# Kernel optimization log

Measured on AMD Instinct MI355X. Metric: run time of the kernel, lower is better.

The kernel has to match this reference:

```python
import jax, jax.numpy as jnp
import numpy as np


def setup_inputs() -> dict:
    key = jax.random.key(0)
    ks = jax.random.split(key, 5)
    B, S, D, H = 2, 2048, 1024, 16
    dk = D // H
    scale = D ** -0.5
    x = jax.random.normal(ks[0], (B, S, D), dtype=jnp.float32)
    W_Q = scale * jax.random.normal(ks[1], (H, D, dk), dtype=jnp.float32)
    W_K = scale * jax.random.normal(ks[2], (H, D, dk), dtype=jnp.float32)
    W_V = scale * jax.random.normal(ks[3], (H, D, dk), dtype=jnp.float32)
    W_O = scale * jax.random.normal(ks[4], (H * dk, D), dtype=jnp.float32)
    return {"x": x, "W_Q": W_Q, "W_K": W_K, "W_V": W_V, "W_O": W_O}


def reference(x, W_Q, W_K, W_V, W_O):
    # x: [B,S,D]; W_Q/W_K/W_V: [H,D,dk]; W_O: [H*dk, D]
    dk = W_Q.shape[-1]
    Q = jnp.einsum('bsd,hdk->bhsk', x, W_Q)
    K = jnp.einsum('bsd,hdk->bhsk', x, W_K)
    V = jnp.einsum('bsd,hdk->bhsk', x, W_V)
    scores = jnp.einsum('bhqk,bhsk->bhqs', Q, K) / jnp.sqrt(jnp.float32(dk))
    attn = jax.nn.softmax(scores, axis=-1)
    heads = jnp.einsum('bhqs,bhsk->bhqk', attn, V)  # [B,H,S,dk]
    B, H, S, _ = heads.shape
    concat = heads.transpose(0, 2, 1, 3).reshape(B, S, H * dk)  # [B,S,H*dk]
    return concat @ W_O
```

## Files before the change

### kernel.cpp

```cpp
#include <hip/hip_runtime.h>

typedef __attribute__((ext_vector_type(8))) short bf16x8;
typedef __attribute__((ext_vector_type(4))) float f32x4;
typedef __attribute__((ext_vector_type(4))) unsigned short u16x4;
typedef unsigned short u16;
typedef unsigned int u32;

static __device__ __forceinline__ u16 f2bf(float f) {
  u32 u = __float_as_uint(f);
  u32 r = (u + 0x7fffu + ((u >> 16) & 1u)) >> 16;
  return (u16)r;
}

static __device__ __forceinline__ u32 cvt_pk(float lo, float hi) {
  u32 r;
  asm("v_cvt_pk_bf16_f32 %0, %1, %2" : "=v"(r) : "v"(lo), "v"(hi));
  return r;
}

#define GLDS16(g, l)                                                        \
  __builtin_amdgcn_global_load_lds(                                         \
      (const __attribute__((address_space(1))) u32*)(g),                    \
      (__attribute__((address_space(3))) u32*)(l), 16, 0, 0)

#define WAIT_VM0() asm volatile("s_waitcnt vmcnt(0)" ::: "memory")
#define RAWBAR() __builtin_amdgcn_s_barrier()

#define SC2F 0.18033688011112042f

__global__ __launch_bounds__(256) void cast_all(const float* __restrict__ x,
                                                const float* __restrict__ wq,
                                                const float* __restrict__ wk,
                                                const float* __restrict__ wv,
                                                const float* __restrict__ wo,
                                                u16* __restrict__ xb,
                                                u16* __restrict__ wqkv,
                                                u16* __restrict__ wot) {
  __shared__ u16 tile[64][66];
  int bid = blockIdx.x, t = threadIdx.x;
  if (bid < 2048) {
    int i = bid * 256 + t;
    const float4* xv = (const float4*)x;
    float4 a = xv[i * 2], b = xv[i * 2 + 1];
    bf16x8 o;
    o[0] = f2bf(a.x); o[1] = f2bf(a.y); o[2] = f2bf(a.z); o[3] = f2bf(a.w);
    o[4] = f2bf(b.x); o[5] = f2bf(b.y); o[6] = f2bf(b.z); o[7] = f2bf(b.w);
    *(bf16x8*)(xb + i * 8) = o;
    return;
  }
  const float* src;
  u16* dstb;
  if (bid < 2816) {
    int id = bid - 2048;
    int dt = id & 15, h = (id >> 4) & 15, sel = id >> 8;
    src = (sel == 0 ? wq : (sel == 1 ? wk : wv)) + h * 65536 + dt * 4096;
    dstb = wqkv + ((size_t)(h * 192 + sel * 64)) * 1024 + dt * 64;
    int r = t >> 4, c4 = (t & 15) * 4;
#pragma unroll
    for (int p = 0; p < 4; ++p) {
      int rr = r + p * 16;
      float4 v = *(const float4*)(src + rr * 64 + c4);
      u16x4 o;
      o[0] = f2bf(v.x); o[1] = f2bf(v.y); o[2] = f2bf(v.z); o[3] = f2bf(v.w);
      *(u16x4*)&tile[rr][c4] = o;
    }
  } else {
    int id = bid - 2816;
    int nt = id & 15, kt = id >> 4;
    src = wo + (size_t)(kt * 64) * 1024 + nt * 64;
    dstb = wot + (size_t)(nt * 64) * 1024 + kt * 64;
    int r = t >> 4, c4 = (t & 15) * 4;
#pragma unroll
    for (int p = 0; p < 4; ++p) {
      int rr = r + p * 16;
      float4 v = *(const float4*)(src + (size_t)rr * 1024 + c4);
      u16x4 o;
      o[0] = f2bf(v.x); o[1] = f2bf(v.y); o[2] = f2bf(v.z); o[3] = f2bf(v.w);
      *(u16x4*)&tile[rr][c4] = o;
    }
  }
  __syncthreads();
  int nn = t >> 3, dc = (t & 7) * 8;
#pragma unroll
  for (int p = 0; p < 2; ++p) {
    int np = nn + p * 32;
    u16x4 a, b2;
#pragma unroll
    for (int i = 0; i < 4; ++i) {
      a[i] = tile[dc + i][np];
      b2[i] = tile[dc + 4 + i][np];
    }
    *(u16x4*)(dstb + (size_t)np * 1024 + dc) = a;
    *(u16x4*)(dstb + (size_t)np * 1024 + dc + 4) = b2;
  }
}

__global__ __launch_bounds__(256) void gemm_qkv(const u16* __restrict__ A,
                                                const u16* __restrict__ Bt,
                                                u16* __restrict__ qkb,
                                                u16* __restrict__ Vt, int M,
                                                int N, int K) {
  const int t = threadIdx.x;
  const int lane = t & 63, w = t >> 6;
  const int lr = lane & 15, lg = lane >> 4;
  const int wr = w >> 1, wc = w & 1;
  int lin = blockIdx.y * gridDim.x + blockIdx.x;
  int bx = 2 * (lin & 7) + ((lin >> 3) & 1);
  int by = lin >> 4;
  const int m0 = by * 128, n0 = bx * 192, head = bx;
  __shared__ __align__(16) u16 SM[40960];
  const int rs = t >> 3, cs = t & 7;
  const int sw = (cs ^ (rs & 7)) * 8;
  const u16* a0 = A + (size_t)(m0 + rs) * K + sw;
  const u16* b0 = Bt + (size_t)(n0 + rs) * K + sw;
  int chk[2];
#pragma unroll
  for (int kk = 0; kk < 2; ++kk) chk[kk] = ((kk * 4 + lg) ^ (lr & 7)) * 8;
  f32x4 acc[4][6] = {};

#define QSTAGE(bb, k0)                                                     \
  {                                                                        \
    _Pragma("unroll") for (int p = 0; p < 4; ++p)                          \
        GLDS16(a0 + (size_t)p * 32 * K + (k0),                             \
               &SM[(bb)*8192 + (p * 256 + t) * 8]);                        \
    _Pragma("unroll") for (int p = 0; p < 6; ++p)                          \
        GLDS16(b0 + (size_t)p * 32 * K + (k0),                             \
               &SM[16384 + (bb)*12288 + (p * 256 + t) * 8]);               \
  }

  QSTAGE(0, 0);
  for (int k0 = 0; k0 < K; k0 += 64) {
    const int bb = (k0 >> 6) & 1;
    WAIT_VM0();
    RAWBAR();
    if (k0 + 64 < K) QSTAGE(bb ^ 1, k0 + 64);
#pragma unroll
    for (int kk = 0; kk < 2; ++kk) {
      bf16x8 a[4], b[6];
#pragma unroll
      for (int m = 0; m < 4; ++m)
        a[m] = *(const bf16x8*)&SM[bb * 8192 + (wr * 64 + m * 16 + lr) * 64 + chk[kk]];
#pragma unroll
      for (int n = 0; n < 6; ++n)
        b[n] = *(const bf16x8*)&SM[16384 + bb * 12288 +
                                   (wc * 96 + n * 16 + lr) * 64 + chk[kk]];
      __builtin_amdgcn_s_setprio(1);
#pragma unroll
      for (int m = 0; m < 4; ++m)
#pragma unroll
        for (int n = 0; n < 6; ++n)
          acc[m][n] =
              __builtin_amdgcn_mfma_f32_16x16x32_bf16(a[m], b[n], acc[m][n], 0, 0, 0);
      __builtin_amdgcn_s_setprio(0);
    }
  }
#undef QSTAGE

#pragma unroll
  for (int m = 0; m < 4; ++m) {
    int rowg = m0 + wr * 64 + m * 16 + lg * 4;
#pragma unroll
    for (int n = 0; n < 6; ++n) {
      int cg = wc * 96 + n * 16 + lr;
      if (cg < 64) {
        int col = head * 64 + cg;
#pragma unroll
        for (int j = 0; j < 4; ++j)
          qkb[(size_t)(rowg + j) * 2048 + col] = f2bf(acc[m][n][j] * SC2F);
      } else if (cg < 128) {
        int col = 1024 + head * 64 + (cg - 64);
#pragma unroll
        for (int j = 0; j < 4; ++j)
          qkb[(size_t)(rowg + j) * 2048 + col] = f2bf(acc[m][n][j]);
      }
    }
  }
  __syncthreads();
  if (wc == 1) {
#pragma unroll
    for (int m = 0; m < 4; ++m)
#pragma unroll
      for (int n = 2; n < 6; ++n) {
        int v = (n - 2) * 16 + lr;
        int s = wr * 64 + m * 16 + lg * 4;
        u16x4 pk;
#pragma unroll
        for (int j = 0; j < 4; ++j) pk[j] = f2bf(acc[m][n][j]);
        *(u16x4*)&SM[v * 136 + s] = pk;
      }
  }
  __syncthreads();
  const int bb2 = m0 >> 11, s0g = m0 & 2047;
  u16* vdst = Vt + ((size_t)(bb2 * 1024 + head * 64)) * 2048 + s0g;
#pragma unroll
  for (int q = 0; q < 4; ++q) {
    int id = q * 256 + t;
    int v = id >> 4, sc = id & 15;
    bf16x8 row = *(const bf16x8*)&SM[v * 136 + sc * 8];
    *(bf16x8*)(vdst + (size_t)v * 2048 + sc * 8) = row;
  }
}

__global__ __launch_bounds__(256) void gemm_out(const u16* __restrict__ A,
                                                const u16* __restrict__ Bt,
                                                float* __restrict__ C, int M,
                                                int N, int K) {
  const int t = threadIdx.x;
  const int lane = t & 63, w = t >> 6;
  const int lr = lane & 15, lg = lane >> 4;
  const int wr = w >> 1, wc = w & 1;
  int lin = blockIdx.y * gridDim.x + blockIdx.x;
  int nwg = gridDim.x * gridDim.y;
  int swz = (lin & 7) * (nwg >> 3) + (lin >> 3);
  int bx = swz % gridDim.x, by = swz / gridDim.x;
  const int m0 = by * 64, n0 = bx * 128;
  __shared__ __align__(16) u16 As[2][64 * 32];
  __shared__ __align__(16) u16 Bs[2][128 * 32];
  const int r0 = t >> 2, cb = (t & 3) * 8;
  const u16* a0 = A + (size_t)(m0 + r0) * K + cb;
  const u16* b0 = Bt + (size_t)(n0 + r0) * K + cb;
  const size_t rowjmp = (size_t)64 * K;
  f32x4 acc[2][4] = {};

#define GSTAGE(bb, k0)                                      \
  {                                                         \
    GLDS16(a0 + (k0), &As[bb][t * 8]);                      \
    GLDS16(b0 + (k0), &Bs[bb][t * 8]);                      \
    GLDS16(b0 + rowjmp + (k0), &Bs[bb][2048 + t * 8]);      \
  }

  GSTAGE(0, 0);
  for (int k0 = 0; k0 < K; k0 += 32) {
    const int bb = (k0 >> 5) & 1;
    WAIT_VM0();
    RAWBAR();
    if (k0 + 32 < K) GSTAGE(bb ^ 1, k0 + 32);
    bf16x8 a[2], b[4];
#pragma unroll
    for (int m = 0; m < 2; ++m)
      a[m] = *(const bf16x8*)&As[bb][(wr * 32 + m * 16 + lr) * 32 + lg * 8];
#pragma unroll
    for (int n = 0; n < 4; ++n)
      b[n] = *(const bf16x8*)&Bs[bb][(wc * 64 + n * 16 + lr) * 32 + lg * 8];
    __builtin_amdgcn_s_setprio(1);
#pragma unroll
    for (int m = 0; m < 2; ++m)
#pragma unroll
      for (int n = 0; n < 4; ++n)
        acc[m][n] =
            __builtin_amdgcn_mfma_f32_16x16x32_bf16(a[m], b[n], acc[m][n], 0, 0, 0);
    __builtin_amdgcn_s_setprio(0);
  }
#undef GSTAGE

#pragma unroll
  for (int m = 0; m < 2; ++m) {
    int rowg = m0 + wr * 32 + m * 16 + lg * 4;
#pragma unroll
    for (int n = 0; n < 4; ++n) {
      int colg = n0 + wc * 64 + n * 16 + lr;
#pragma unroll
      for (int j = 0; j < 4; ++j)
        C[(size_t)(rowg + j) * N + colg] = acc[m][n][j];
    }
  }
}

__global__ __launch_bounds__(256, 2) void attn(const u16* __restrict__ qkb,
                                               const u16* __restrict__ vtb,
                                               u16* __restrict__ hb) {
  const int t = threadIdx.x, lane = t & 63, w = t >> 6;
  const int lr = lane & 15, lg = lane >> 4;
  int lin = blockIdx.x;
  int swz2 = (lin & 7) * 64 + (lin >> 3);
  int qi = swz2 & 15, bh = swz2 >> 4;
  int b = bh >> 4, h = bh & 15;
  int q0 = qi * 128;
  __shared__ __align__(16) u16 Ks[2][128 * 64];
  __shared__ __align__(16) u16 Vts[2][64 * 128];
  __shared__ __align__(16) u32 Ps[4][2][512];

  bf16x8 qf[2][2];
#pragma unroll
  for (int g = 0; g < 2; ++g) {
    const u16* qb =
        qkb + (size_t)(b * 2048 + q0 + w * 32 + g * 16 + lr) * 2048 + h * 64;
    qf[g][0] = *(const bf16x8*)(qb + lg * 8);
    qf[g][1] = *(const bf16x8*)(qb + 32 + lg * 8);
  }
  bf16x8 ones;
#pragma unroll
  for (int i = 0; i < 8; ++i) ones[i] = (short)0x3F80;

  f32x4 oacc[2][4] = {};
  f32x4 le0 = {}, le1 = {};
  float mrun0 = -1e30f, mrun1 = -1e30f;

  int chk[2], chv[4];
#pragma unroll
  for (int kk = 0; kk < 2; ++kk) chk[kk] = ((kk * 4 + lg) ^ (lr & 7)) * 8;
#pragma unroll
  for (int kk = 0; kk < 4; ++kk) chv[kk] = ((kk * 4 + lg) ^ lr) * 8;
  const int xw = (lr & 7) << 2;

  const int rk = t >> 3, ck = t & 7;
  const int rv = t >> 4, cv = t & 15;
  const u16* Kg = qkb + (size_t)(b * 2048) * 2048 + 1024 + h * 64;
  const u16* Vg = vtb + (size_t)(b * 1024 + h * 64) * 2048;
  const u16* kp0 = Kg + (size_t)rk * 2048 + ((ck ^ (rk & 7)) * 8);
  const u16* vp0 = Vg + (size_t)rv * 2048 + ((cv ^ (rv & 15)) * 8);
  u32* Pw0 = &Ps[w][0][0];
  u32* Pw1 = &Ps[w][1][0];

#define ASTAGE(bb, tv)                                 \
  {                                                    \
    const u16* kp = kp0 + (size_t)(tv)*262144;         \
    const u16* vp = vp0 + (tv)*128;                    \
    GLDS16(kp, &Ks[bb][t * 8]);                        \
    GLDS16(kp + 65536, &Ks[bb][2048 + t * 8]);         \
    GLDS16(kp + 131072, &Ks[bb][4096 + t * 8]);        \
    GLDS16(kp + 196608, &Ks[bb][6144 + t * 8]);        \
    GLDS16(vp, &Vts[bb][t * 8]);                       \
    GLDS16(vp + 32768, &Vts[bb][2048 + t * 8]);        \
    GLDS16(vp + 65536, &Vts[bb][4096 + t * 8]);        \
    GLDS16(vp + 98304, &Vts[bb][6144 + t * 8]);        \
  }

  ASTAGE(0, 0);
  for (int tv = 0; tv < 16; ++tv) {
    const int bb = tv & 1;
    WAIT_VM0();
    RAWBAR();
    if (tv < 15) ASTAGE(bb ^ 1, tv + 1);

    f32x4 s0[8], s1[8];
#pragma unroll
    for (int n = 0; n < 8; ++n) {
      s0[n] = (f32x4){0.f, 0.f, 0.f, 0.f};
      s1[n] = (f32x4){0.f, 0.f, 0.f, 0.f};
    }
    __builtin_amdgcn_s_setprio(1);
#pragma unroll
    for (int kk = 0; kk < 2; ++kk)
#pragma unroll
      for (int n = 0; n < 8; ++n) {
        bf16x8 kf = *(const bf16x8*)&Ks[bb][n * 1024 + lr * 64 + chk[kk]];
        s0[n] = __builtin_amdgcn_mfma_f32_16x16x32_bf16(kf, qf[0][kk], s0[n], 0, 0, 0);
        s1[n] = __builtin_amdgcn_mfma_f32_16x16x32_bf16(kf, qf[1][kk], s1[n], 0, 0, 0);
      }
    __builtin_amdgcn_s_setprio(0);

    if ((tv & 3) == 0) {
      float t0[8], t1[8];
#pragma unroll
      for (int n = 0; n < 8; ++n) {
        t0[n] = fmaxf(fmaxf(s0[n][0], s0[n][1]), fmaxf(s0[n][2], s0[n][3]));
        t1[n] = fmaxf(fmaxf(s1[n][0], s1[n][1]), fmaxf(s1[n][2], s1[n][3]));
      }
      float pm0 = fmaxf(fmaxf(fmaxf(t0[0], t0[1]), fmaxf(t0[2], t0[3])),
                        fmaxf(fmaxf(t0[4], t0[5]), fmaxf(t0[6], t0[7])));
      float pm1 = fmaxf(fmaxf(fmaxf(t1[0], t1[1]), fmaxf(t1[2], t1[3])),
                        fmaxf(fmaxf(t1[4], t1[5]), fmaxf(t1[6], t1[7])));
      pm0 = fmaxf(pm0, __shfl_xor(pm0, 16));
      pm0 = fmaxf(pm0, __shfl_xor(pm0, 32));
      pm1 = fmaxf(pm1, __shfl_xor(pm1, 16));
      pm1 = fmaxf(pm1, __shfl_xor(pm1, 32));

      if (__any(fmaxf(pm0 - mrun0, pm1 - mrun1) > 8.0f)) {
        {
          float mn = fmaxf(mrun0, pm0);
          float al = __builtin_amdgcn_exp2f(mrun0 - mn);
          float alj[4];
#pragma unroll
          for (int j = 0; j < 4; ++j) alj[j] = __shfl(al, 4 * lg + j);
#pragma unroll
          for (int j = 0; j < 4; ++j) le0[j] *= alj[j];
#pragma unroll
          for (int n = 0; n < 4; ++n)
#pragma unroll
            for (int j = 0; j < 4; ++j) oacc[0][n][j] *= alj[j];
          mrun0 = mn;
        }
        {
          float mn = fmaxf(mrun1, pm1);
          float al = __builtin_amdgcn_exp2f(mrun1 - mn);
          float alj[4];
#pragma unroll
          for (int j = 0; j < 4; ++j) alj[j] = __shfl(al, 4 * lg + j);
#pragma unroll
          for (int j = 0; j < 4; ++j) le1[j] *= alj[j];
#pragma unroll
          for (int n = 0; n < 4; ++n)
#pragma unroll
            for (int j = 0; j < 4; ++j) oacc[1][n][j] *= alj[j];
          mrun1 = mn;
        }
      }
    }

#pragma unroll
    for (int n = 0; n < 4; ++n) {
      float v0 = __builtin_amdgcn_exp2f(s0[n][0] - mrun0);
      float v1 = __builtin_amdgcn_exp2f(s0[n][1] - mrun0);
      float v2 = __builtin_amdgcn_exp2f(s0[n][2] - mrun0);
      float v3 = __builtin_amdgcn_exp2f(s0[n][3] - mrun0);
      Pw0[lr * 32 + ((8 * n + 2 * lg) ^ xw)] = cvt_pk(v0, v1);
      Pw0[lr * 32 + ((8 * n + 2 * lg + 1) ^ xw)] = cvt_pk(v2, v3);
      float u0 = __builtin_amdgcn_exp2f(s1[n][0] - mrun1);
      float u1 = __builtin_amdgcn_exp2f(s1[n][1] - mrun1);
      float u2 = __builtin_amdgcn_exp2f(s1[n][2] - mrun1);
      float u3 = __builtin_amdgcn_exp2f(s1[n][3] - mrun1);
      Pw1[lr * 32 + ((8 * n + 2 * lg) ^ xw)] = cvt_pk(u0, u1);
      Pw1[lr * 32 + ((8 * n + 2 * lg + 1) ^ xw)] = cvt_pk(u2, u3);
    }
    __builtin_amdgcn_s_setprio(1);
#pragma unroll
    for (int kk = 0; kk < 2; ++kk) {
      bf16x8 pa0 = *(const bf16x8*)&Pw0[lr * 32 + ((16 * kk + 4 * lg) ^ xw)];
      bf16x8 pa1 = *(const bf16x8*)&Pw1[lr * 32 + ((16 * kk + 4 * lg) ^ xw)];
      le0 = __builtin_amdgcn_mfma_f32_16x16x32_bf16(pa0, ones, le0, 0, 0, 0);
      le1 = __builtin_amdgcn_mfma_f32_16x16x32_bf16(pa1, ones, le1, 0, 0, 0);
#pragma unroll
      for (int n = 0; n < 4; ++n) {
        bf16x8 vf = *(const bf16x8*)&Vts[bb][n * 2048 + lr * 128 + chv[kk]];
        oacc[0][n] = __builtin_amdgcn_mfma_f32_16x16x32_bf16(pa0, vf, oacc[0][n], 0, 0, 0);
        oacc[1][n] = __builtin_amdgcn_mfma_f32_16x16x32_bf16(pa1, vf, oacc[1][n], 0, 0, 0);
      }
    }
    __builtin_amdgcn_s_setprio(0);
#pragma unroll
    for (int n = 4; n < 8; ++n) {
      float v0 = __builtin_amdgcn_exp2f(s0[n][0] - mrun0);
      float v1 = __builtin_amdgcn_exp2f(s0[n][1] - mrun0);
      float v2 = __builtin_amdgcn_exp2f(s0[n][2] - mrun0);
      float v3 = __builtin_amdgcn_exp2f(s0[n][3] - mrun0);
      Pw0[lr * 32 + ((8 * (n - 4) + 2 * lg) ^ xw)] = cvt_pk(v0, v1);
      Pw0[lr * 32 + ((8 * (n - 4) + 2 * lg + 1) ^ xw)] = cvt_pk(v2, v3);
      float u0 = __builtin_amdgcn_exp2f(s1[n][0] - mrun1);
      float u1 = __builtin_amdgcn_exp2f(s1[n][1] - mrun1);
      float u2 = __builtin_amdgcn_exp2f(s1[n][2] - mrun1);
      float u3 = __builtin_amdgcn_exp2f(s1[n][3] - mrun1);
      Pw1[lr * 32 + ((8 * (n - 4) + 2 * lg) ^ xw)] = cvt_pk(u0, u1);
      Pw1[lr * 32 + ((8 * (n - 4) + 2 * lg + 1) ^ xw)] = cvt_pk(u2, u3);
    }
    __builtin_amdgcn_s_setprio(1);
#pragma unroll
    for (int kk = 2; kk < 4; ++kk) {
      bf16x8 pa0 = *(const bf16x8*)&Pw0[lr * 32 + ((16 * (kk - 2) + 4 * lg) ^ xw)];
      bf16x8 pa1 = *(const bf16x8*)&Pw1[lr * 32 + ((16 * (kk - 2) + 4 * lg) ^ xw)];
      le0 = __builtin_amdgcn_mfma_f32_16x16x32_bf16(pa0, ones, le0, 0, 0, 0);
      le1 = __builtin_amdgcn_mfma_f32_16x16x32_bf16(pa1, ones, le1, 0, 0, 0);
#pragma unroll
      for (int n = 0; n < 4; ++n) {
        bf16x8 vf = *(const bf16x8*)&Vts[bb][n * 2048 + lr * 128 + chv[kk]];
        oacc[0][n] = __builtin_amdgcn_mfma_f32_16x16x32_bf16(pa0, vf, oacc[0][n], 0, 0, 0);
        oacc[1][n] = __builtin_amdgcn_mfma_f32_16x16x32_bf16(pa1, vf, oacc[1][n], 0, 0, 0);
      }
    }
    __builtin_amdgcn_s_setprio(0);
  }
#undef ASTAGE

  float rj0[4], rj1[4];
#pragma unroll
  for (int j = 0; j < 4; ++j) {
    rj0[j] = __builtin_amdgcn_rcpf(le0[j]);
    rj1[j] = __builtin_amdgcn_rcpf(le1[j]);
  }
  int row0 = b * 2048 + q0 + w * 32 + lg * 4;
#pragma unroll
  for (int n = 0; n < 4; ++n) {
    int col = h * 64 + n * 16 + lr;
#pragma unroll
    for (int j = 0; j < 4; ++j) {
      hb[(size_t)(row0 + j) * 1024 + col] = f2bf(oacc[0][n][j] * rj0[j]);
      hb[(size_t)(row0 + 16 + j) * 1024 + col] = f2bf(oacc[1][n][j] * rj1[j]);
    }
  }
}

extern "C" void kernel_launch(void* const* d_in, const int* in_sizes, int n_in,
                              void* d_out, int out_size, void* d_ws,
                              size_t ws_size, hipStream_t stream) {
  const float* x = (const float*)d_in[0];
  const float* wq = (const float*)d_in[1];
  const float* wk = (const float*)d_in[2];
  const float* wv = (const float*)d_in[3];
  const float* wo = (const float*)d_in[4];

  u16* xb = (u16*)d_ws;
  u16* wqkv = xb + 4 * 1024 * 1024;
  u16* wot = wqkv + 3 * 1024 * 1024;
  u16* qkb = wot + 1024 * 1024;
  u16* vtb = qkb + 8 * 1024 * 1024;
  u16* hb = vtb + 4 * 1024 * 1024;

  cast_all<<<3072, 256, 0, stream>>>(x, wq, wk, wv, wo, xb, wqkv, wot);
  gemm_qkv<<<dim3(16, 32), 256, 0, stream>>>(xb, wqkv, qkb, vtb, 4096, 3072, 1024);
  attn<<<512, 256, 0, stream>>>(qkb, vtb, hb);
  gemm_out<<<dim3(8, 64), 256, 0, stream>>>(hb, wot, (float*)d_out, 4096, 1024, 1024);
}
```

Baseline: 111.4 us.

## Use triple-buffered K=32 stages with partial vmcnt waits in QKV GEMM

New measurement: 112.8 us. Within noise of the previous version (+1.3%).

```diff
diff --git a/kernel.cpp b/kernel.cpp
--- a/kernel.cpp
+++ b/kernel.cpp
@@ -23,6 +23,7 @@
       (const __attribute__((address_space(1))) u32*)(g),                    \
       (__attribute__((address_space(3))) u32*)(l), 16, 0, 0)
 
+#define WAIT_VM5() asm volatile("s_waitcnt vmcnt(5)" ::: "memory")
 #define WAIT_VM0() asm volatile("s_waitcnt vmcnt(0)" ::: "memory")
 #define RAWBAR() __builtin_amdgcn_s_barrier()
 
@@ -108,51 +109,49 @@
   int bx = 2 * (lin & 7) + ((lin >> 3) & 1);
   int by = lin >> 4;
   const int m0 = by * 128, n0 = bx * 192, head = bx;
-  __shared__ __align__(16) u16 SM[40960];
-  const int rs = t >> 3, cs = t & 7;
-  const int sw = (cs ^ (rs & 7)) * 8;
-  const u16* a0 = A + (size_t)(m0 + rs) * K + sw;
-  const u16* b0 = Bt + (size_t)(n0 + rs) * K + sw;
-  int chk[2];
-#pragma unroll
-  for (int kk = 0; kk < 2; ++kk) chk[kk] = ((kk * 4 + lg) ^ (lr & 7)) * 8;
+  __shared__ __align__(16) u16 SM[30720];
+  const int ra = t >> 2, ca = (t & 3) * 8;
+  const u16* a0 = A + (size_t)(m0 + ra) * K + ca;
+  const u16* b0 = Bt + (size_t)(n0 + ra) * K + ca;
   f32x4 acc[4][6] = {};
 
-#define QSTAGE(bb, k0)                                                     \
-  {                                                                        \
-    _Pragma("unroll") for (int p = 0; p < 4; ++p)                          \
-        GLDS16(a0 + (size_t)p * 32 * K + (k0),                             \
-               &SM[(bb)*8192 + (p * 256 + t) * 8]);                        \
-    _Pragma("unroll") for (int p = 0; p < 6; ++p)                          \
-        GLDS16(b0 + (size_t)p * 32 * K + (k0),                             \
-               &SM[16384 + (bb)*12288 + (p * 256 + t) * 8]);               \
+#define QSTAGE(sb, k0)                                                      \
+  {                                                                         \
+    GLDS16(a0 + (k0), &SM[(sb)*10240 + t * 8]);                             \
+    GLDS16(a0 + (size_t)64 * K + (k0), &SM[(sb)*10240 + 2048 + t * 8]);     \
+    GLDS16(b0 + (k0), &SM[(sb)*10240 + 4096 + t * 8]);                      \
+    GLDS16(b0 + (size_t)64 * K + (k0), &SM[(sb)*10240 + 6144 + t * 8]);     \
+    GLDS16(b0 + (size_t)128 * K + (k0), &SM[(sb)*10240 + 8192 + t * 8]);    \
   }
 
   QSTAGE(0, 0);
-  for (int k0 = 0; k0 < K; k0 += 64) {
-    const int bb = (k0 >> 6) & 1;
-    WAIT_VM0();
+  QSTAGE(1, 32);
+  for (int k0 = 0; k0 < K; k0 += 32) {
+    const int st = k0 >> 5;
+    const int sb = st % 3;
+    if (k0 + 32 < K) {
+      WAIT_VM5();
+    } else {
+      WAIT_VM0();
+    }
     RAWBAR();
-    if (k0 + 64 < K) QSTAGE(bb ^ 1, k0 + 64);
-#pragma unroll
-    for (int kk = 0; kk < 2; ++kk) {
-      bf16x8 a[4], b[6];
-#pragma unroll
-      for (int m = 0; m < 4; ++m)
-        a[m] = *(const bf16x8*)&SM[bb * 8192 + (wr * 64 + m * 16 + lr) * 64 + chk[kk]];
+    if (k0 + 64 < K) QSTAGE((st + 2) % 3, k0 + 64);
+    bf16x8 a[4], b[6];
+#pragma unroll
+    for (int m = 0; m < 4; ++m)
+      a[m] = *(const bf16x8*)&SM[sb * 10240 + (wr * 64 + m * 16 + lr) * 32 + lg * 8];
+#pragma unroll
+    for (int n = 0; n < 6; ++n)
+      b[n] = *(const bf16x8*)&SM[sb * 10240 + 4096 +
+                                 (wc * 96 + n * 16 + lr) * 32 + lg * 8];
+    __builtin_amdgcn_s_setprio(1);
+#pragma unroll
+    for (int m = 0; m < 4; ++m)
 #pragma unroll
       for (int n = 0; n < 6; ++n)
-        b[n] = *(const bf16x8*)&SM[16384 + bb * 12288 +
-                                   (wc * 96 + n * 16 + lr) * 64 + chk[kk]];
-      __builtin_amdgcn_s_setprio(1);
-#pragma unroll
-      for (int m = 0; m < 4; ++m)
-#pragma unroll
-        for (int n = 0; n < 6; ++n)
-          acc[m][n] =
-              __builtin_amdgcn_mfma_f32_16x16x32_bf16(a[m], b[n], acc[m][n], 0, 0, 0);
-      __builtin_amdgcn_s_setprio(0);
-    }
+        acc[m][n] =
+            __builtin_amdgcn_mfma_f32_16x16x32_bf16(a[m], b[n], acc[m][n], 0, 0, 0);
+    __builtin_amdgcn_s_setprio(0);
   }
 #undef QSTAGE
 
```
